# Optimization experiments

Measured on AMD Instinct MI355X. Metric: run time of the kernel, lower is better.

The kernel has to match this reference:

```python
import jax, jax.numpy as jnp
import numpy as np
from jax import lax

RATIOS = (0.5, 1.0, 2.0)
SCALES = (8, 16, 32)
BASE_SIZE = 16
FEAT_STRIDE = 16
IMG_H = IMG_W = 800.0
PRE_NMS = 6000   # test-phase pre-NMS top-k
POST_NMS = 300   # test-phase proposals kept
NMS_THRESH = 0.7
MIN_SIZE = 16.0  # 16 * img_scale(=1.0)


def _anchor_base():
    ab = []
    for r in RATIOS:
        for s in SCALES:
            h = BASE_SIZE * s * np.sqrt(r)
            w = BASE_SIZE * s * np.sqrt(1.0 / r)
            cy = cx = BASE_SIZE / 2.0
            ab.append([cy - h / 2, cx - w / 2, cy + h / 2, cx + w / 2])
    return np.asarray(ab, dtype=np.float32)  # [9, 4] (y1,x1,y2,x2)


def _all_anchors(fh, fw):
    base = _anchor_base()
    sy = np.arange(fh, dtype=np.float32) * FEAT_STRIDE
    sx = np.arange(fw, dtype=np.float32) * FEAT_STRIDE
    shift = np.stack(np.meshgrid(sy, sx, indexing='ij'), axis=-1)  # [fh,fw,2]
    shift4 = np.concatenate([shift, shift], axis=-1)               # [fh,fw,4]
    anchors = shift4[:, :, None, :] + base[None, None]             # [fh,fw,9,4]
    return jnp.asarray(anchors.reshape(-1, 4))                     # [fh*fw*9,4]


def _conv(x, w, b, pad):
    y = lax.conv_general_dilated(x, w, (1, 1), [(pad, pad), (pad, pad)],
                                 dimension_numbers=('NCHW', 'OIHW', 'NCHW'))
    return y + b[None, :, None, None]


def _iou_one_vs_all(box, boxes):
    ty1 = jnp.maximum(box[0], boxes[:, 0])
    tx1 = jnp.maximum(box[1], boxes[:, 1])
    ty2 = jnp.minimum(box[2], boxes[:, 2])
    tx2 = jnp.minimum(box[3], boxes[:, 3])
    inter = jnp.maximum(ty2 - ty1, 0.0) * jnp.maximum(tx2 - tx1, 0.0)
    a1 = (box[2] - box[0]) * (box[3] - box[1])
    a2 = (boxes[:, 2] - boxes[:, 0]) * (boxes[:, 3] - boxes[:, 1])
    return inter / (a1 + a2 - inter + 1e-9)


def _nms(boxes, scores):
    # fixed-iteration greedy NMS: pick argmax, suppress IoU > thresh
    def body(s, _):
        i = jnp.argmax(s)
        v = s[i] > -jnp.inf
        ov = _iou_one_vs_all(boxes[i], boxes)
        s = jnp.where(ov > NMS_THRESH, -jnp.inf, s)
        return s, (i, v)
    _, (idxs, valid) = lax.scan(body, scores, None, length=POST_NMS)
    return idxs, valid


def _propose(score, loc, anchors):
    # decode (loc2bbox)
    ha = anchors[:, 2] - anchors[:, 0]
    wa = anchors[:, 3] - anchors[:, 1]
    cya = anchors[:, 0] + 0.5 * ha
    cxa = anchors[:, 1] + 0.5 * wa
    dy, dx, dh, dw = loc[:, 0], loc[:, 1], loc[:, 2], loc[:, 3]
    cy = dy * ha + cya
    cx = dx * wa + cxa
    h = jnp.exp(dh) * ha
    w = jnp.exp(dw) * wa
    y1 = jnp.clip(cy - 0.5 * h, 0.0, IMG_H)
    x1 = jnp.clip(cx - 0.5 * w, 0.0, IMG_W)
    y2 = jnp.clip(cy + 0.5 * h, 0.0, IMG_H)
    x2 = jnp.clip(cx + 0.5 * w, 0.0, IMG_W)
    boxes = jnp.stack([y1, x1, y2, x2], axis=-1)
    keep = ((y2 - y1) >= MIN_SIZE) & ((x2 - x1) >= MIN_SIZE)
    score = jnp.where(keep, score, -jnp.inf)
    topv, topi = lax.top_k(score, PRE_NMS)
    b = boxes[topi]
    keep_idx, valid = _nms(b, topv)
    rois = b[keep_idx] * valid[:, None].astype(b.dtype)  # zero-pad invalid slots
    return rois, valid


def setup_inputs() -> dict:
    key = jax.random.key(0)
    ks = jax.random.split(key, 4)
    std = 0.01
    x = jax.random.normal(ks[0], (8, 512, 50, 50), dtype=jnp.float32)
    W_share = std * jax.random.normal(ks[1], (512, 512, 3, 3), dtype=jnp.float32)
    W_cls = std * jax.random.normal(ks[2], (18, 512, 1, 1), dtype=jnp.float32)
    W_reg = std * jax.random.normal(ks[3], (36, 512, 1, 1), dtype=jnp.float32)
    return {
        'x': x,
        'W_share': W_share, 'b_share': jnp.zeros((512,), jnp.float32),
        'W_cls': W_cls, 'b_cls': jnp.zeros((18,), jnp.float32),
        'W_reg': W_reg, 'b_reg': jnp.zeros((36,), jnp.float32),
    }


def reference(x, W_share, b_share, W_cls, b_cls, W_reg, b_reg):
    B, _, fh, fw = x.shape
    anchors = _all_anchors(fh, fw)  # [fh*fw*9, 4]
    shared = jax.nn.relu(_conv(x, W_share, b_share, 1))
    cls = _conv(shared, W_cls, b_cls, 0)                      # [B,18,h,w]
    cls = cls.transpose(0, 2, 3, 1).reshape(B, fh, fw, 9, 2)
    cls = jax.nn.softmax(cls, axis=4).reshape(B, -1, 2)       # [B,N,2]
    reg = _conv(shared, W_reg, b_reg, 0)                      # [B,36,h,w]
    reg = reg.transpose(0, 2, 3, 1).reshape(B, -1, 4)         # [B,N,4]
    fg_scores = cls[..., 1]
    rois, valid = jax.vmap(lambda s, l: _propose(s, l, anchors))(fg_scores, reg)
    roi_id = jnp.broadcast_to(jnp.arange(B, dtype=jnp.int32)[:, None], valid.shape)
    roi_id = roi_id * valid.astype(jnp.int32)
    return reg, cls, rois, roi_id, anchors
```

## Files before the change

kernel.cpp:

```cpp
#include <hip/hip_runtime.h>
#include <cmath>

#define NANCH 22500

#define OUT_REG   0
#define OUT_CLS   720000
#define OUT_ROIS  1080000
#define OUT_ROIID 1089600
#define OUT_ANCH  1092000

__device__ __forceinline__ unsigned keyOf(float f) {
  unsigned u = __float_as_uint(f);
  return (u & 0x80000000u) ? ~u : (u | 0x80000000u);
}

__device__ __forceinline__ float cr_expf(float x) {
  return (float)exp((double)x);
}

__device__ __forceinline__ void anchor4(int a, int yy, int xx,
    float& y1, float& x1, float& y2, float& x2) {
  int ri = a / 3, si = a - ri * 3;
  double r = (ri == 0) ? 0.5 : ((ri == 1) ? 1.0 : 2.0);
  double s = (si == 0) ? 8.0 : ((si == 1) ? 16.0 : 32.0);
  double h = 16.0 * s * sqrt(r);
  double w = 16.0 * s * sqrt(1.0 / r);
  float sy = (float)(yy * 16), sx = (float)(xx * 16);
  y1 = sy + (float)(8.0 - 0.5 * h);
  x1 = sx + (float)(8.0 - 0.5 * w);
  y2 = sy + (float)(8.0 + 0.5 * h);
  x2 = sx + (float)(8.0 + 0.5 * w);
}

__global__ __launch_bounds__(256, 3) void k_conv3x3(
    const float* __restrict__ x, const float* __restrict__ Wsh,
    const float* __restrict__ bsh, double* __restrict__ sh)
{
  __shared__ float  xs[16 * 312];
  __shared__ double wl[16 * 64];
  const int t = threadIdx.x;
  const int px0 = blockIdx.x * 128, co0 = blockIdx.y * 64, b = blockIdx.z;
  const int pxg = t & 15, cog = t >> 4;
  const int r0 = px0 / 50;
  int off[8], pp[8];
  #pragma unroll
  for (int j = 0; j < 8; ++j) {
    int p = px0 + pxg + 16 * j;
    pp[j] = p;
    int q = (p < 2500) ? p : 2499;
    int r = q / 50, c = q - r * 50;
    off[j] = (r - r0 + 1) * 52 + c + 1;
  }
  double acc[8][4];
  #pragma unroll
  for (int j = 0; j < 8; ++j)
    #pragma unroll
    for (int i = 0; i < 4; ++i) acc[j][i] = 0.0;

  for (int cc = 0; cc < 32; ++cc) {
    const int cibase = cc * 16;
    for (int idx = t; idx < 16 * 312; idx += 256) {
      int ci = idx / 312;
      int rem = idx - ci * 312;
      int rr = rem / 52, cs = rem - rr * 52;
      int gr = r0 - 1 + rr, gc = cs - 1;
      float v = 0.f;
      if (gr >= 0 && gr < 50 && gc >= 0 && gc < 50)
        v = x[(((size_t)b * 512 + cibase + ci) * 50 + gr) * 50 + gc];
      xs[idx] = v;
    }
    for (int tap = 0; tap < 9; ++tap) {
      for (int idx = t; idx < 1024; idx += 256) {
        int ci = idx >> 6, co = idx & 63;
        wl[idx] = (double)Wsh[(size_t)(co0 + co) * 4608 + (size_t)(cibase + ci) * 9 + tap];
      }
      __syncthreads();
      const int dt = ((tap / 3) - 1) * 52 + (tap % 3) - 1;
      #pragma unroll
      for (int ci = 0; ci < 16; ++ci) {
        const double w0 = wl[ci * 64 + cog * 4 + 0];
        const double w1 = wl[ci * 64 + cog * 4 + 1];
        const double w2 = wl[ci * 64 + cog * 4 + 2];
        const double w3 = wl[ci * 64 + cog * 4 + 3];
        double a[8];
        #pragma unroll
        for (int j = 0; j < 8; ++j)
          a[j] = (double)xs[ci * 312 + off[j] + dt];
        #pragma unroll
        for (int j = 0; j < 8; ++j) {
          acc[j][0] = fma(a[j], w0, acc[j][0]);
          acc[j][1] = fma(a[j], w1, acc[j][1]);
          acc[j][2] = fma(a[j], w2, acc[j][2]);
          acc[j][3] = fma(a[j], w3, acc[j][3]);
        }
      }
      __syncthreads();
    }
  }
  #pragma unroll
  for (int i = 0; i < 4; ++i) {
    int co = co0 + cog * 4 + i;
    float bv = bsh[co];
    #pragma unroll
    for (int j = 0; j < 8; ++j) {
      if (pp[j] < 2500) {
        float v = (float)acc[j][i] + bv;
        v = fmaxf(v, 0.f);
        sh[((size_t)b * 512 + co) * 2500 + pp[j]] = (double)v;
      }
    }
  }
}

__global__ __launch_bounds__(256) void k_heads(
    const double* __restrict__ sh, const float* __restrict__ Wc,
    const float* __restrict__ bc, const float* __restrict__ Wr,
    const float* __restrict__ br, float* __restrict__ out,
    float* __restrict__ scores, float* __restrict__ boxes)
{
#pragma clang fp contract(off)
  __shared__ double xs2[32][64];
  __shared__ float wcl[56][32];
  __shared__ float accs[64][56];
  const int t = threadIdx.x;
  const int p0 = blockIdx.x * 64, b = blockIdx.y;
  const int px = t & 63, wg = t >> 6;
  double acc[14];
  #pragma unroll
  for (int j = 0; j < 14; ++j) acc[j] = 0.0;

  for (int cc = 0; cc < 16; ++cc) {
    for (int idx = t; idx < 2048; idx += 256) {
      int ci = idx >> 6, pl = idx & 63;
      int p = p0 + pl;
      xs2[ci][pl] = (p < 2500) ? sh[((size_t)b * 512 + cc * 32 + ci) * 2500 + p] : 0.0;
    }
    for (int idx = t; idx < 1792; idx += 256) {
      int co = idx >> 5, ci = idx & 31;
      float v = 0.f;
      if (co < 18) v = Wc[co * 512 + cc * 32 + ci];
      else if (co < 54) v = Wr[(co - 18) * 512 + cc * 32 + ci];
      wcl[co][ci] = v;
    }
    __syncthreads();
    for (int ci = 0; ci < 32; ++ci) {
      double a = xs2[ci][px];
      #pragma unroll
      for (int j = 0; j < 14; ++j) acc[j] += a * (double)wcl[wg * 14 + j][ci];
    }
    __syncthreads();
  }
  #pragma unroll
  for (int j = 0; j < 14; ++j) {
    int co = wg * 14 + j;
    float bias = (co < 18) ? bc[co] : ((co < 54) ? br[co - 18] : 0.f);
    accs[px][co] = (float)acc[j] + bias;
  }
  __syncthreads();

  for (int e = t; e < 64 * 18; e += 256) {
    int pxl = e / 18, c = e - pxl * 18;
    int p = p0 + pxl;
    if (p < 2500) {
      int a = c >> 1, k = c & 1;
      float l0 = accs[pxl][2 * a];
      float l1 = accs[pxl][2 * a + 1];
      float mm = fmaxf(l0, l1);
      float e0 = cr_expf(l0 - mm);
      float e1 = cr_expf(l1 - mm);
      float sum = e0 + e1;
      out[OUT_CLS + ((size_t)b * NANCH + (size_t)p * 9 + a) * 2 + k] = (k ? e1 : e0) / sum;
    }
  }
  for (int e = t; e < 64 * 36; e += 256) {
    int pxl = e / 36, c = e - pxl * 36;
    int p = p0 + pxl;
    if (p < 2500)
      out[((size_t)b * NANCH + (size_t)p * 9 + (c >> 2)) * 4 + (c & 3)] = accs[pxl][18 + c];
  }
  for (int e = t; e < 64 * 9; e += 256) {
    int pxl = e / 9, a = e - pxl * 9;
    int p = p0 + pxl;
    if (p < 2500) {
      float l0 = accs[pxl][2 * a];
      float l1 = accs[pxl][2 * a + 1];
      float mm = fmaxf(l0, l1);
      float e0 = cr_expf(l0 - mm);
      float e1 = cr_expf(l1 - mm);
      float fg = e1 / (e0 + e1);
      float dy = accs[pxl][18 + a * 4 + 0];
      float dx = accs[pxl][18 + a * 4 + 1];
      float dh = accs[pxl][18 + a * 4 + 2];
      float dw = accs[pxl][18 + a * 4 + 3];
      int yy = p / 50, xx = p - yy * 50;
      float ay1, ax1, ay2, ax2;
      anchor4(a, yy, xx, ay1, ax1, ay2, ax2);
      float ha  = ay2 - ay1;
      float wa2 = ax2 - ax1;
      float cya = ay1 + 0.5f * ha;
      float cxa = ax1 + 0.5f * wa2;
      float cy = dy * ha;  cy = cy + cya;
      float cx = dx * wa2; cx = cx + cxa;
      float hh = cr_expf(dh); hh = hh * ha;
      float ww = cr_expf(dw); ww = ww * wa2;
      float t1;
      t1 = 0.5f * hh; float y1 = cy - t1; y1 = fminf(fmaxf(y1, 0.f), 800.f);
      t1 = 0.5f * ww; float x1 = cx - t1; x1 = fminf(fmaxf(x1, 0.f), 800.f);
      t1 = 0.5f * hh; float y2 = cy + t1; y2 = fminf(fmaxf(y2, 0.f), 800.f);
      t1 = 0.5f * ww; float x2 = cx + t1; x2 = fminf(fmaxf(x2, 0.f), 800.f);
      bool keep = (y2 - y1 >= 16.f) && (x2 - x1 >= 16.f);
      size_t gi = (size_t)b * NANCH + (size_t)p * 9 + a;
      scores[gi] = keep ? fg : -INFINITY;
      *(float4*)(boxes + gi * 4) = make_float4(y1, x1, y2, x2);
    }
  }
}

__global__ __launch_bounds__(256) void k_anchors(float* __restrict__ out) {
  int i = blockIdx.x * 256 + threadIdx.x;
  if (i < NANCH) {
    int p = i / 9, a = i - p * 9;
    int yy = p / 50, xx = p - yy * 50;
    float y1, x1, y2, x2;
    anchor4(a, yy, xx, y1, x1, y2, x2);
    *(float4*)(out + OUT_ANCH + (size_t)i * 4) = make_float4(y1, x1, y2, x2);
  }
}

__global__ __launch_bounds__(1024) void k_nms(
    const float* __restrict__ scores, const float* __restrict__ boxes,
    float* __restrict__ out)
{
#pragma clang fp contract(off)
  const int b = blockIdx.x;
  const float* s = scores + (size_t)b * NANCH;
  const float* bx = boxes + (size_t)b * NANCH * 4;
  const int t = threadIdx.x;
  const int lane = t & 63, wid = t >> 6;
  __shared__ float cscore[6000];
  __shared__ float4 cbox[6000];
  __shared__ unsigned sHist[256];
  __shared__ unsigned sScan[17];
  __shared__ float wred_s[16];
  __shared__ int wred_e[16];
  __shared__ unsigned sPrefix, sKr, sG;
  __shared__ float sWinS;
  __shared__ int sWinE;

  for (int e = t; e < 6000; e += 1024) {
    cscore[e] = -INFINITY;
    cbox[e] = make_float4(0.f, 0.f, 0.f, 0.f);
  }
  if (t == 0) { sPrefix = 0u; sKr = 6000u; sG = 0u; }
  __syncthreads();

  for (int pass = 0; pass < 4; ++pass) {
    const int shift = 24 - 8 * pass;
    if (t < 256) sHist[t] = 0u;
    __syncthreads();
    const unsigned pref = sPrefix;
    const unsigned himask = (pass == 0) ? 0u : (0xFFFFFFFFu << (shift + 8));
    for (int i = t; i < NANCH; i += 1024) {
      unsigned key = keyOf(s[i]);
      if ((key & himask) == pref) atomicAdd(&sHist[(key >> shift) & 255u], 1u);
    }
    __syncthreads();
    if (t == 0) {
      unsigned Kr = sKr, acc = 0; int dsel = 0;
      for (int d = 255; d >= 0; --d) {
        unsigned c = sHist[d];
        if (acc + c >= Kr) { dsel = d; break; }
        acc += c;
      }
      sPrefix = pref | ((unsigned)dsel << shift);
      sKr = Kr - acc;
    }
    __syncthreads();
  }
  const unsigned cut = sPrefix;

  unsigned cg = 0;
  for (int i = t; i < NANCH; i += 1024)
    if (keyOf(s[i]) > cut) cg++;
  atomicAdd(&sG, cg);
  __syncthreads();
  const unsigned Gc = sG;
  const unsigned R = (Gc < 6000u) ? (6000u - Gc) : 0u;

  unsigned run_gt = 0, run_eq = 0;
  for (int chunk = 0; chunk < 22; ++chunk) {
    int i = (chunk << 10) + t;
    float sv = 0.f; unsigned key = 0u;
    if (i < NANCH) { sv = s[i]; key = keyOf(sv); }
    unsigned item = (i < NANCH) ? ((key > cut) ? 0x10000u : ((key == cut) ? 1u : 0u)) : 0u;
    unsigned inc = item;
    #pragma unroll
    for (int d = 1; d < 64; d <<= 1) {
      unsigned n = __shfl_up(inc, d, 64);
      if (lane >= d) inc += n;
    }
    if (lane == 63) sScan[wid] = inc;
    __syncthreads();
    if (t == 0) {
      unsigned a2 = 0;
      for (int k = 0; k < 16; ++k) { unsigned tmp = sScan[k]; sScan[k] = a2; a2 += tmp; }
      sScan[16] = a2;
    }
    __syncthreads();
    unsigned excl = inc - item + sScan[wid];
    unsigned total = sScan[16];
    __syncthreads();
    unsigned gt_b = run_gt + (excl >> 16);
    unsigned eq_b = run_eq + (excl & 0xFFFFu);
    bool sel = ((item >> 16) != 0u) || (((item & 0xFFFFu) != 0u) && (eq_b < R));
    if (sel) {
      unsigned pos = gt_b + (eq_b < R ? eq_b : R);
      if (pos < 6000u) {
        cscore[pos] = sv;
        cbox[pos] = *(const float4*)(bx + (size_t)i * 4);
      }
    }
    run_gt += (total >> 16); run_eq += (total & 0xFFFFu);
  }
  __syncthreads();

  float sreg[6]; float4 breg[6];
  #pragma unroll
  for (int j = 0; j < 6; ++j) {
    int e = t + (j << 10);
    if (e < 6000) {
      sreg[j] = cscore[e];
      breg[j] = cbox[e];
    } else {
      sreg[j] = -INFINITY;
      breg[j] = make_float4(0.f, 0.f, 0.f, 0.f);
    }
  }
  __syncthreads();

  for (int it = 0; it < 300; ++it) {
    float bs = sreg[0]; int be = t;
    #pragma unroll
    for (int j = 1; j < 6; ++j) {
      if (sreg[j] > bs) { bs = sreg[j]; be = t + (j << 10); }
    }
    #pragma unroll
    for (int d = 1; d < 64; d <<= 1) {
      float os = __shfl_xor(bs, d);
      int oe = __shfl_xor(be, d);
      if (os > bs || (os == bs && oe < be)) { bs = os; be = oe; }
    }
    if (lane == 0) { wred_s[wid] = bs; wred_e[wid] = be; }
    __syncthreads();
    if (t == 0) {
      float ws0 = wred_s[0]; int we0 = wred_e[0];
      for (int k = 1; k < 16; ++k) {
        float s2 = wred_s[k]; int e2 = wred_e[k];
        if (s2 > ws0 || (s2 == ws0 && e2 < we0)) { ws0 = s2; we0 = e2; }
      }
      sWinS = ws0; sWinE = we0;
    }
    __syncthreads();
    const float wsc = sWinS; const int we = sWinE;
    const float4 wb = cbox[we];
    const bool valid = (wsc > -INFINITY);
    if (t == 0) {
      const float m = valid ? 1.f : 0.f;
      size_t ro = OUT_ROIS + ((size_t)b * 300 + it) * 4;
      out[ro + 0] = wb.x * m; out[ro + 1] = wb.y * m;
      out[ro + 2] = wb.z * m; out[ro + 3] = wb.w * m;
      out[OUT_ROIID + (size_t)b * 300 + it] = valid ? (float)b : 0.f;
    }
    {
      const float a1 = (wb.z - wb.x) * (wb.w - wb.y);
      #pragma unroll
      for (int j = 0; j < 6; ++j) {
        float ty1 = fmaxf(wb.x, breg[j].x);
        float tx1 = fmaxf(wb.y, breg[j].y);
        float ty2 = fminf(wb.z, breg[j].z);
        float tx2 = fminf(wb.w, breg[j].w);
        float inter = fmaxf(ty2 - ty1, 0.f) * fmaxf(tx2 - tx1, 0.f);
        float a2 = (breg[j].z - breg[j].x) * (breg[j].w - breg[j].y);
        float ov = inter / (a1 + a2 - inter + 1e-9f);
        if (ov > 0.7f) sreg[j] = -INFINITY;
      }
    }
    __syncthreads();
  }
}

extern "C" void kernel_launch(void* const* d_in, const int* in_sizes, int n_in,
                              void* d_out, int out_size, void* d_ws, size_t ws_size,
                              hipStream_t stream) {
  (void)in_sizes; (void)n_in; (void)out_size;
  const size_t need = (size_t)10240000 * 8 + (size_t)(180000 + 720000) * 4;
  if (ws_size < need) return;
  const float* x   = (const float*)d_in[0];
  const float* Wsh = (const float*)d_in[1];
  const float* bsh = (const float*)d_in[2];
  const float* Wc  = (const float*)d_in[3];
  const float* bc  = (const float*)d_in[4];
  const float* Wr  = (const float*)d_in[5];
  const float* br  = (const float*)d_in[6];
  float* out = (float*)d_out;
  double* sh = (double*)d_ws;
  float* scores = (float*)(sh + 10240000);
  float* boxes  = scores + 180000;

  hipLaunchKernelGGL(k_conv3x3, dim3(20, 8, 8), dim3(256), 0, stream, x, Wsh, bsh, sh);
  hipLaunchKernelGGL(k_heads,   dim3(40, 8),    dim3(256), 0, stream, sh, Wc, bc, Wr, br, out, scores, boxes);
  hipLaunchKernelGGL(k_anchors, dim3(88),       dim3(256), 0, stream, out);
  hipLaunchKernelGGL(k_nms,     dim3(8),        dim3(1024), 0, stream, scores, boxes, out);
}
```

Baseline: 3.847 ms.

## Widen conv3x3 output-channel tile to 128 and store shared activations as float

The 3x3 conv block now computes 128 output channels instead of 64, so each thread holds an 8x8 double accumulator tile. This halves how often the input tile is reloaded per output channel and halves the grid's y dimension. The shared activation buffer changes from double to float, which halves its memory traffic, and k_heads converts back to double on load. Gather offsets for the input tile are precomputed once per thread. The larger register tile lowers occupancy (launch bounds 3→2) and may spill.

```diff
diff --git a/kernel.cpp b/kernel.cpp
--- a/kernel.cpp
+++ b/kernel.cpp
@@ -32,14 +32,14 @@
   x2 = sx + (float)(8.0 + 0.5 * w);
 }
 
-__global__ __launch_bounds__(256, 3) void k_conv3x3(
+__global__ __launch_bounds__(256, 2) void k_conv3x3(
     const float* __restrict__ x, const float* __restrict__ Wsh,
-    const float* __restrict__ bsh, double* __restrict__ sh)
+    const float* __restrict__ bsh, float* __restrict__ sh)
 {
   __shared__ float  xs[16 * 312];
-  __shared__ double wl[16 * 64];
+  __shared__ double wl[16 * 128];
   const int t = threadIdx.x;
-  const int px0 = blockIdx.x * 128, co0 = blockIdx.y * 64, b = blockIdx.z;
+  const int px0 = blockIdx.x * 128, co0 = blockIdx.y * 128, b = blockIdx.z;
   const int pxg = t & 15, cog = t >> 4;
   const int r0 = px0 / 50;
   int off[8], pp[8];
@@ -51,69 +51,78 @@
     int r = q / 50, c = q - r * 50;
     off[j] = (r - r0 + 1) * 52 + c + 1;
   }
-  double acc[8][4];
-  #pragma unroll
-  for (int j = 0; j < 8; ++j)
-    #pragma unroll
-    for (int i = 0; i < 4; ++i) acc[j][i] = 0.0;
-
-  for (int cc = 0; cc < 32; ++cc) {
-    const int cibase = cc * 16;
-    for (int idx = t; idx < 16 * 312; idx += 256) {
+  int srcOff[20];
+  #pragma unroll
+  for (int k = 0; k < 20; ++k) {
+    int idx = t + 256 * k;
+    srcOff[k] = -1;
+    if (idx < 4992) {
       int ci = idx / 312;
       int rem = idx - ci * 312;
       int rr = rem / 52, cs = rem - rr * 52;
       int gr = r0 - 1 + rr, gc = cs - 1;
-      float v = 0.f;
       if (gr >= 0 && gr < 50 && gc >= 0 && gc < 50)
-        v = x[(((size_t)b * 512 + cibase + ci) * 50 + gr) * 50 + gc];
-      xs[idx] = v;
+        srcOff[k] = ci * 2500 + gr * 50 + gc;
+    }
+  }
+  double acc[8][8];
+  #pragma unroll
+  for (int j = 0; j < 8; ++j)
+    #pragma unroll
+    for (int i = 0; i < 8; ++i) acc[j][i] = 0.0;
+
+  for (int cc = 0; cc < 32; ++cc) {
+    const int cibase = cc * 16;
+    const float* xc = x + (size_t)(b * 512 + cibase) * 2500;
+    #pragma unroll
+    for (int k = 0; k < 20; ++k) {
+      int idx = t + 256 * k;
+      if (idx < 4992)
+        xs[idx] = (srcOff[k] >= 0) ? xc[srcOff[k]] : 0.f;
     }
     for (int tap = 0; tap < 9; ++tap) {
-      for (int idx = t; idx < 1024; idx += 256) {
-        int ci = idx >> 6, co = idx & 63;
+      #pragma unroll
+      for (int k = 0; k < 8; ++k) {
+        int idx = t + 256 * k;
+        int ci = idx >> 7, co = idx & 127;
         wl[idx] = (double)Wsh[(size_t)(co0 + co) * 4608 + (size_t)(cibase + ci) * 9 + tap];
       }
       __syncthreads();
       const int dt = ((tap / 3) - 1) * 52 + (tap % 3) - 1;
       #pragma unroll
       for (int ci = 0; ci < 16; ++ci) {
-        const double w0 = wl[ci * 64 + cog * 4 + 0];
-        const double w1 = wl[ci * 64 + cog * 4 + 1];
-        const double w2 = wl[ci * 64 + cog * 4 + 2];
-        const double w3 = wl[ci * 64 + cog * 4 + 3];
+        double w[8];
+        #pragma unroll
+        for (int i = 0; i < 8; ++i) w[i] = wl[ci * 128 + cog * 8 + i];
         double a[8];
         #pragma unroll
         for (int j = 0; j < 8; ++j)
           a[j] = (double)xs[ci * 312 + off[j] + dt];
         #pragma unroll
-        for (int j = 0; j < 8; ++j) {
-          acc[j][0] = fma(a[j], w0, acc[j][0]);
-          acc[j][1] = fma(a[j], w1, acc[j][1]);
-          acc[j][2] = fma(a[j], w2, acc[j][2]);
-          acc[j][3] = fma(a[j], w3, acc[j][3]);
-        }
+        for (int j = 0; j < 8; ++j)
+          #pragma unroll
+          for (int i = 0; i < 8; ++i)
+            acc[j][i] = fma(a[j], w[i], acc[j][i]);
       }
       __syncthreads();
     }
   }
   #pragma unroll
-  for (int i = 0; i < 4; ++i) {
-    int co = co0 + cog * 4 + i;
+  for (int i = 0; i < 8; ++i) {
+    int co = co0 + cog * 8 + i;
     float bv = bsh[co];
     #pragma unroll
     for (int j = 0; j < 8; ++j) {
       if (pp[j] < 2500) {
         float v = (float)acc[j][i] + bv;
-        v = fmaxf(v, 0.f);
-        sh[((size_t)b * 512 + co) * 2500 + pp[j]] = (double)v;
+        sh[((size_t)b * 512 + co) * 2500 + pp[j]] = fmaxf(v, 0.f);
       }
     }
   }
 }
 
 __global__ __launch_bounds__(256) void k_heads(
-    const double* __restrict__ sh, const float* __restrict__ Wc,
+    const float* __restrict__ sh, const float* __restrict__ Wc,
     const float* __restrict__ bc, const float* __restrict__ Wr,
     const float* __restrict__ br, float* __restrict__ out,
     float* __restrict__ scores, float* __restrict__ boxes)
@@ -133,7 +142,7 @@
     for (int idx = t; idx < 2048; idx += 256) {
       int ci = idx >> 6, pl = idx & 63;
       int p = p0 + pl;
-      xs2[ci][pl] = (p < 2500) ? sh[((size_t)b * 512 + cc * 32 + ci) * 2500 + p] : 0.0;
+      xs2[ci][pl] = (p < 2500) ? (double)sh[((size_t)b * 512 + cc * 32 + ci) * 2500 + p] : 0.0;
     }
     for (int idx = t; idx < 1792; idx += 256) {
       int co = idx >> 5, ci = idx & 31;
@@ -393,7 +402,7 @@
                               void* d_out, int out_size, void* d_ws, size_t ws_size,
                               hipStream_t stream) {
   (void)in_sizes; (void)n_in; (void)out_size;
-  const size_t need = (size_t)10240000 * 8 + (size_t)(180000 + 720000) * 4;
+  const size_t need = (size_t)(10240000 + 180000 + 720000) * 4;
   if (ws_size < need) return;
   const float* x   = (const float*)d_in[0];
   const float* Wsh = (const float*)d_in[1];
@@ -403,11 +412,12 @@
   const float* Wr  = (const float*)d_in[5];
   const float* br  = (const float*)d_in[6];
   float* out = (float*)d_out;
-  double* sh = (double*)d_ws;
-  float* scores = (float*)(sh + 10240000);
-  float* boxes  = scores + 180000;
-
-  hipLaunchKernelGGL(k_conv3x3, dim3(20, 8, 8), dim3(256), 0, stream, x, Wsh, bsh, sh);
+  float* ws  = (float*)d_ws;
+  float* sh     = ws;
+  float* scores = ws + 10240000;
+  float* boxes  = ws + 10420000;
+
+  hipLaunchKernelGGL(k_conv3x3, dim3(20, 4, 8), dim3(256), 0, stream, x, Wsh, bsh, sh);
   hipLaunchKernelGGL(k_heads,   dim3(40, 8),    dim3(256), 0, stream, sh, Wc, bc, Wr, br, out, scores, boxes);
   hipLaunchKernelGGL(k_anchors, dim3(88),       dim3(256), 0, stream, out);
   hipLaunchKernelGGL(k_nms,     dim3(8),        dim3(1024), 0, stream, scores, boxes, out);
```

Result: slower. 4.252 ms (+10.5%).
